# Optimization experiments

Measured on AMD Instinct MI355X. Metric: run time of the kernel, lower is better.

## Reference

```python
import jax, jax.numpy as jnp
import numpy as np
from jax import lax

B, T, HW = 8, 32, 128
D, NH, DEPTH, DFF = 384, 6, 6, 1536
PR = PC = 4
P = PR * PC
EPS = 1e-5


def _ln(x, g, b):
    mu = x.mean(-1, keepdims=True)
    v = ((x - mu) ** 2).mean(-1, keepdims=True)
    return (x - mu) / jnp.sqrt(v + EPS) * g + b


def _conv2d(x, w, s, p):
    return lax.conv_general_dilated(x, w, (s, s), [(p, p), (p, p)],
                                    dimension_numbers=('NCHW', 'OIHW', 'NCHW'))


def _bn(x, g, b, m, v):
    inv = g / jnp.sqrt(v + EPS)
    return x * inv[:, None, None] + (b - m * inv)[:, None, None]


def _gelu(x):
    return jax.nn.gelu(x, approximate=False)


def _forward(frames, conv1_w, bn1_g, bn1_b, bn1_m, bn1_v,
             conv2_w, bn2_g, bn2_b, bn2_m, bn2_v,
             conv3_w, bn3_g, bn3_b, bn3_m, bn3_v, proj_w,
             dw_w, dw_b, pw_w, pw_b, tnorm_g, tnorm_b,
             frame_pos, patch_pos, cls_token, cls_pos,
             qkv_w, qkv_b, out_w, out_b, ln1_g, ln1_b, ln2_g, ln2_b,
             ffn_w1, ffn_b1, ffn_w2, ffn_b2,
             head_ln_g, head_ln_b, head_w1, head_b1, head_w2, head_b2):
    b, t = frames.shape[0], frames.shape[1]
    # ---- FrameEncoder (eval-mode BN) ----
    x = frames.reshape(b * t, 1, HW, HW)
    x = _gelu(_bn(_conv2d(x, conv1_w, 2, 2), bn1_g, bn1_b, bn1_m, bn1_v))
    x = _gelu(_bn(_conv2d(x, conv2_w, 2, 1), bn2_g, bn2_b, bn2_m, bn2_v))
    x = _gelu(_bn(_conv2d(x, conv3_w, 2, 1), bn3_g, bn3_b, bn3_m, bn3_v))
    n, c, hh, ww = x.shape
    # adaptive avg pool (16,16)->(4,4) is an exact 4x4 mean pool
    x = x.reshape(n, c, PR, hh // PR, PC, ww // PC).mean(axis=(3, 5))
    x = jnp.einsum('oc,nchw->nohw', proj_w[:, :, 0, 0], x)  # 1x1 conv proj
    tokens = x.reshape(n, D, P).transpose(0, 2, 1).reshape(b, t, P, D)
    # ---- TemporalConvBlock (per-patch sequences) ----
    tc = tokens.transpose(0, 2, 1, 3).reshape(b * P, t, D)
    out = tc.transpose(0, 2, 1)  # [N, D, t]
    for i, dil in enumerate((1, 2)):
        pad = dil * (3 - 1) // 2
        h = lax.conv_general_dilated(out, dw_w[i], (1,), [(pad, pad)],
                                     rhs_dilation=(dil,), feature_group_count=D,
                                     dimension_numbers=('NCH', 'OIH', 'NCH'))
        h = _gelu(h + dw_b[i][None, :, None])
        h = jnp.einsum('oi,nit->not', pw_w[i], h) + pw_b[i][None, :, None]
        out = h + out
    out = out.transpose(0, 2, 1)
    tc = _ln(out + tc, tnorm_g, tnorm_b)
    tokens = tc.reshape(b, P, t, D).transpose(0, 2, 1, 3)
    # ---- positional + cls ----
    fp = frame_pos[:t].transpose(1, 0, 2)[:, :, None, :]  # [1,t,1,D]
    pp = patch_pos[:, None, :, :]                          # [1,1,P,D]
    tok = (tokens + fp + pp).reshape(b, t * P, D)
    cls = cls_token + cls_pos
    tok = jnp.concatenate([jnp.broadcast_to(cls, (b, 1, D)), tok], axis=1)
    S = t * P + 1
    # ---- block-structured additive mask (faithful to _build_causal_mask) ----
    ids = jnp.repeat(jnp.arange(t), P)
    neg = jnp.finfo(jnp.float32).min
    base = jnp.where(ids[None, :] < ids[:, None], neg, 0.0)
    mask = jnp.zeros((S, S), jnp.float32).at[1:, 1:].set(base).at[1:, 0].set(neg)
    # ---- pre-norm transformer encoder ----
    hd = D // NH
    scale = 1.0 / jnp.sqrt(jnp.float32(hd))
    x = tok
    for i in range(DEPTH):
        h = _ln(x, ln1_g[i], ln1_b[i])
        qkv = h @ qkv_w[i].T + qkv_b[i]
        q, k, v = jnp.split(qkv, 3, axis=-1)
        q = q.reshape(b, S, NH, hd).transpose(0, 2, 1, 3)
        k = k.reshape(b, S, NH, hd).transpose(0, 2, 1, 3)
        v = v.reshape(b, S, NH, hd).transpose(0, 2, 1, 3)
        scores = jnp.einsum('bhqd,bhkd->bhqk', q, k) * scale + mask
        a = jax.nn.softmax(scores, axis=-1)
        o = jnp.einsum('bhqk,bhkd->bhqd', a, v).transpose(0, 2, 1, 3).reshape(b, S, D)
        x = x + (o @ out_w[i].T + out_b[i])
        h2 = _ln(x, ln2_g[i], ln2_b[i])
        x = x + _gelu(h2 @ ffn_w1[i].T + ffn_b1[i]) @ ffn_w2[i].T + ffn_b2[i]
    # ---- coord head ----
    pooled = x[:, 0]
    h = _ln(pooled, head_ln_g, head_ln_b)
    h = _gelu(h @ head_w1.T + head_b1)
    coords = jax.nn.sigmoid(h @ head_w2.T + head_b2)
    return coords


def setup_inputs():
    ks = iter(jax.random.split(jax.random.key(0), 64))

    def r(shape, s):
        return jax.random.normal(next(ks), shape, jnp.float32) * s

    inp = {}
    inp['frames'] = jax.random.normal(next(ks), (B, T, 1, HW, HW), jnp.float32)
    inp['conv1_w'] = r((32, 1, 5, 5), 0.2)
    inp['bn1_g'] = jnp.ones(32); inp['bn1_b'] = jnp.zeros(32)
    inp['bn1_m'] = r((32,), 0.1)
    inp['bn1_v'] = jax.random.uniform(next(ks), (32,), jnp.float32, 0.5, 1.5)
    inp['conv2_w'] = r((64, 32, 3, 3), 0.1)
    inp['bn2_g'] = jnp.ones(64); inp['bn2_b'] = jnp.zeros(64)
    inp['bn2_m'] = r((64,), 0.1)
    inp['bn2_v'] = jax.random.uniform(next(ks), (64,), jnp.float32, 0.5, 1.5)
    inp['conv3_w'] = r((128, 64, 3, 3), 0.07)
    inp['bn3_g'] = jnp.ones(128); inp['bn3_b'] = jnp.zeros(128)
    inp['bn3_m'] = r((128,), 0.1)
    inp['bn3_v'] = jax.random.uniform(next(ks), (128,), jnp.float32, 0.5, 1.5)
    inp['proj_w'] = r((D, 128, 1, 1), 0.08)
    inp['dw_w'] = r((2, D, 1, 3), 0.3)
    inp['dw_b'] = jnp.zeros((2, D))
    inp['pw_w'] = r((2, D, D), 0.05)
    inp['pw_b'] = jnp.zeros((2, D))
    inp['tnorm_g'] = jnp.ones(D); inp['tnorm_b'] = jnp.zeros(D)
    inp['frame_pos'] = r((T, 1, D), 0.02)
    inp['patch_pos'] = r((1, P, D), 0.02)
    inp['cls_token'] = jnp.zeros((1, 1, D))
    inp['cls_pos'] = r((1, 1, D), 0.02)
    inp['qkv_w'] = r((DEPTH, 3 * D, D), 0.02)
    inp['qkv_b'] = jnp.zeros((DEPTH, 3 * D))
    inp['out_w'] = r((DEPTH, D, D), 0.02)
    inp['out_b'] = jnp.zeros((DEPTH, D))
    inp['ln1_g'] = jnp.ones((DEPTH, D)); inp['ln1_b'] = jnp.zeros((DEPTH, D))
    inp['ln2_g'] = jnp.ones((DEPTH, D)); inp['ln2_b'] = jnp.zeros((DEPTH, D))
    inp['ffn_w1'] = r((DEPTH, DFF, D), 0.02)
    inp['ffn_b1'] = jnp.zeros((DEPTH, DFF))
    inp['ffn_w2'] = r((DEPTH, D, DFF), 0.02)
    inp['ffn_b2'] = jnp.zeros((DEPTH, D))
    inp['head_ln_g'] = jnp.ones(D); inp['head_ln_b'] = jnp.zeros(D)
    inp['head_w1'] = r((D, D), 0.02); inp['head_b1'] = jnp.zeros(D)
    inp['head_w2'] = r((2, D), 0.02); inp['head_b2'] = jnp.zeros(2)
    return inp


def reference(frames, conv1_w, bn1_g, bn1_b, bn1_m, bn1_v,
              conv2_w, bn2_g, bn2_b, bn2_m, bn2_v,
              conv3_w, bn3_g, bn3_b, bn3_m, bn3_v, proj_w,
              dw_w, dw_b, pw_w, pw_b, tnorm_g, tnorm_b,
              frame_pos, patch_pos, cls_token, cls_pos,
              qkv_w, qkv_b, out_w, out_b, ln1_g, ln1_b, ln2_g, ln2_b,
              ffn_w1, ffn_b1, ffn_w2, ffn_b2,
              head_ln_g, head_ln_b, head_w1, head_b1, head_w2, head_b2):
    return _forward(frames, conv1_w, bn1_g, bn1_b, bn1_m, bn1_v,
                    conv2_w, bn2_g, bn2_b, bn2_m, bn2_v,
                    conv3_w, bn3_g, bn3_b, bn3_m, bn3_v, proj_w,
                    dw_w, dw_b, pw_w, pw_b, tnorm_g, tnorm_b,
                    frame_pos, patch_pos, cls_token, cls_pos,
                    qkv_w, qkv_b, out_w, out_b, ln1_g, ln1_b, ln2_g, ln2_b,
                    ffn_w1, ffn_b1, ffn_w2, ffn_b2,
                    head_ln_g, head_ln_b, head_w1, head_b1, head_w2, head_b2)
```

## Files before the change

kernel.cpp:

```cpp
#include <hip/hip_runtime.h>
#include <hip/hip_fp16.h>
#include <cstddef>

#define EPSV 1e-5f
#define SPLITS 4

typedef _Float16 f16;
typedef _Float16 f16x8 __attribute__((ext_vector_type(8)));
typedef float f32x4v __attribute__((ext_vector_type(4)));

__device__ __forceinline__ float gelu_f(float x) {
    return 0.5f * x * (1.0f + erff(x * 0.7071067811865476f));
}

__device__ __forceinline__ float gelu_fast(float x) {
    float x2 = x * x;
    float z = x * fmaf(0.10296103f, x2, 2.3025851f);
    float e = exp2f(z);
    float r = __builtin_amdgcn_rcpf(e + 1.0f);
    return fmaf(-x, r, x);
}

__global__ __launch_bounds__(256) void cvt_all_kernel(
    const float* __restrict__ p0, const float* __restrict__ p1,
    const float* __restrict__ p2, const float* __restrict__ p3,
    const float* __restrict__ p4, const float* __restrict__ p5,
    f16* __restrict__ dst)
{
    const int n = 10960896;
    for (int i = blockIdx.x * 256 + threadIdx.x; i < n; i += gridDim.x * 256) {
        const float* s; int off;
        if      (i <   49152) { s = p0; off = i; }
        else if (i <  344064) { s = p1; off = i -   49152; }
        else if (i < 2998272) { s = p2; off = i -  344064; }
        else if (i < 3883008) { s = p3; off = i - 2998272; }
        else if (i < 7421952) { s = p4; off = i - 3883008; }
        else                  { s = p5; off = i - 7421952; }
        dst[i] = (f16)s[off];
    }
}

__global__ __launch_bounds__(256) void conv_w_reorder_kernel(
    const float* __restrict__ w, f16* __restrict__ out, int CO, int CI)
{
    int n = CO * CI * 9;
    for (int i = blockIdx.x * 256 + threadIdx.x; i < n; i += gridDim.x * 256) {
        int t = i % 9; int r = i / 9;
        int ci = r % CI; int co = r / CI;
        out[(size_t)co * CI * 9 + t * CI + ci] = (f16)w[i];
    }
}

__global__ __launch_bounds__(256) void conv1_w_prep_kernel(
    const float* __restrict__ w, const float* __restrict__ g,
    const float* __restrict__ vr, f16* __restrict__ wB)
{
    int i = blockIdx.x * 256 + threadIdx.x;
    if (i >= 1024) return;
    int co = i >> 5, k = i & 31;
    float inv = g[co] * rsqrtf(vr[co] + EPSV);
    wB[i] = (f16)((k < 25) ? w[co * 25 + k] * inv : 0.f);
}

__global__ __launch_bounds__(256) void conv1_mfma_kernel(
    const float* __restrict__ in, const f16* __restrict__ wB,
    const float* __restrict__ bt, const float* __restrict__ mn,
    const float* __restrict__ g, const float* __restrict__ vr,
    f16* __restrict__ out)
{
    __shared__ __align__(16) f16 inpH[35 * 36 + 8];
    __shared__ __align__(16) f16 Bs[32 * 32];
    int bid = blockIdx.x;
    int n = bid >> 4; int tile = bid & 15;
    int ty0 = (tile >> 2) * 16, tx0 = (tile & 3) * 16;
    int t = threadIdx.x;
    const float* ip = in + (size_t)n * 16384;
    for (int e = t; e < 35 * 36; e += 256) {
        int r = e / 36, c = e - r * 36;
        int iy = ty0 * 2 - 2 + r, ix = tx0 * 2 - 2 + c;
        float v = ((unsigned)iy < 128u && (unsigned)ix < 128u && c < 35) ? ip[iy * 128 + ix] : 0.f;
        inpH[e] = (f16)v;
    }
    if (t < 128) {
        int row = t >> 2, seg = (t & 3) * 8;
        *(uint4*)(&Bs[row * 32 + seg]) = *(const uint4*)(wB + row * 32 + seg);
    }
    __syncthreads();
    int w = t >> 6, lane = t & 63;
    int l15 = lane & 15, gq = lane >> 4;
    f16x8 afr[4];
    #pragma unroll
    for (int i = 0; i < 4; i++) {
        int mt = 4 * w + i;
        f16 tmp[8];
        #pragma unroll
        for (int e = 0; e < 8; e++) {
            int kk = 8 * gq + e; if (kk > 24) kk = 24;
            int ky = kk / 5, kx = kk - ky * 5;
            tmp[e] = inpH[(2 * mt + ky) * 36 + 2 * l15 + kx];
        }
        afr[i] = *(f16x8*)tmp;
    }
    f16x8 bfr[2];
    bfr[0] = *(const f16x8*)(&Bs[l15 * 32 + 8 * gq]);
    bfr[1] = *(const f16x8*)(&Bs[(16 + l15) * 32 + 8 * gq]);
    f32x4v zero = {0.f, 0.f, 0.f, 0.f};
    f32x4v acc[4][2];
    #pragma unroll
    for (int i = 0; i < 4; i++) { acc[i][0] = zero; acc[i][1] = zero; }
    #pragma unroll
    for (int i = 0; i < 4; i++) {
        acc[i][0] = __builtin_amdgcn_mfma_f32_16x16x32_f16(afr[i], bfr[0], acc[i][0], 0, 0, 0);
        acc[i][1] = __builtin_amdgcn_mfma_f32_16x16x32_f16(afr[i], bfr[1], acc[i][1], 0, 0, 0);
    }
    float beta[2];
    #pragma unroll
    for (int nt = 0; nt < 2; nt++) {
        int co = nt * 16 + l15;
        float inv = g[co] * rsqrtf(vr[co] + EPSV);
        beta[nt] = bt[co] - mn[co] * inv;
    }
    #pragma unroll
    for (int i = 0; i < 4; i++) {
        int y = ty0 + 4 * w + i;
        #pragma unroll
        for (int q = 0; q < 4; q++) {
            int x = tx0 + 4 * gq + q;
            size_t ob = (((size_t)n * 64 + y) * 64 + x) * 32;
            #pragma unroll
            for (int nt = 0; nt < 2; nt++) {
                int co = nt * 16 + l15;
                out[ob + co] = (f16)gelu_fast(acc[i][nt][q] + beta[nt]);
            }
        }
    }
}

template<int CI, int HI, int CO>
__global__ __launch_bounds__(256) void convg_kernel(
    const f16* __restrict__ in, const f16* __restrict__ wr_,
    const float* __restrict__ g, const float* __restrict__ bt,
    const float* __restrict__ mn, const float* __restrict__ vr,
    f16* __restrict__ out)
{
    constexpr int HO = HI / 2;
    constexpr int HOB = (HO == 32) ? 5 : 4;
    constexpr int K = 9 * CI;
    __shared__ __align__(16) f16 As[64 * 40];
    __shared__ __align__(16) f16 Bs[64 * 40];
    int tid = threadIdx.x;
    int bm = blockIdx.x * 64;
    int bn = blockIdx.y * 64;
    int lrow = tid >> 2, lseg = tid & 3;
    int w = tid >> 6, lane = tid & 63;
    int wr = (w >> 1) * 32, wc = (w & 1) * 32;
    int l15 = lane & 15, l4 = lane >> 4;
    int gp = bm + lrow;
    int pn = gp >> (2 * HOB);
    int prem = gp & ((1 << (2 * HOB)) - 1);
    int oy = prem >> HOB, ox = prem & (HO - 1);

    f32x4v zero = {0.f, 0.f, 0.f, 0.f};
    f32x4v acc[2][2];
    acc[0][0] = zero; acc[0][1] = zero; acc[1][0] = zero; acc[1][1] = zero;

    auto loadTile = [&](int k0, uint4& av, uint4& bv) {
        int tap = k0 / CI;
        int cio = k0 - tap * CI;
        int ky = tap / 3, kx = tap - ky * 3;
        int iy = oy * 2 - 1 + ky, ix = ox * 2 - 1 + kx;
        av = make_uint4(0u, 0u, 0u, 0u);
        if ((unsigned)iy < (unsigned)HI && (unsigned)ix < (unsigned)HI)
            av = *(const uint4*)(in + (((size_t)(pn * HI + iy)) * HI + ix) * CI + cio + lseg * 8);
        bv = *(const uint4*)(wr_ + (size_t)(bn + lrow) * K + k0 + lseg * 8);
    };

    uint4 ra, rb;
    loadTile(0, ra, rb);
    for (int k0 = 0; k0 < K; k0 += 32) {
        __syncthreads();
        *(uint4*)(&As[lrow * 40 + lseg * 8]) = ra;
        *(uint4*)(&Bs[lrow * 40 + lseg * 8]) = rb;
        if (k0 + 32 < K) loadTile(k0 + 32, ra, rb);
        __syncthreads();
        f16x8 a0 = *(const f16x8*)(&As[(wr + l15) * 40 + l4 * 8]);
        f16x8 a1 = *(const f16x8*)(&As[(wr + 16 + l15) * 40 + l4 * 8]);
        f16x8 b0 = *(const f16x8*)(&Bs[(wc + l15) * 40 + l4 * 8]);
        f16x8 b1 = *(const f16x8*)(&Bs[(wc + 16 + l15) * 40 + l4 * 8]);
        acc[0][0] = __builtin_amdgcn_mfma_f32_16x16x32_f16(a0, b0, acc[0][0], 0, 0, 0);
        acc[0][1] = __builtin_amdgcn_mfma_f32_16x16x32_f16(a0, b1, acc[0][1], 0, 0, 0);
        acc[1][0] = __builtin_amdgcn_mfma_f32_16x16x32_f16(a1, b0, acc[1][0], 0, 0, 0);
        acc[1][1] = __builtin_amdgcn_mfma_f32_16x16x32_f16(a1, b1, acc[1][1], 0, 0, 0);
    }
    float inv[2], beta[2];
    #pragma unroll
    for (int ni = 0; ni < 2; ni++) {
        int col = bn + wc + ni * 16 + l15;
        float iv = g[col] * rsqrtf(vr[col] + EPSV);
        inv[ni] = iv; beta[ni] = bt[col] - mn[col] * iv;
    }
    #pragma unroll
    for (int mi = 0; mi < 2; mi++) {
        #pragma unroll
        for (int q = 0; q < 4; q++) {
            int pixel = bm + wr + mi * 16 + l4 * 4 + q;
            #pragma unroll
            for (int ni = 0; ni < 2; ni++) {
                int col = bn + wc + ni * 16 + l15;
                float v = acc[mi][ni][q] * inv[ni] + beta[ni];
                out[(size_t)pixel * CO + col] = (f16)gelu_fast(v);
            }
        }
    }
}

__global__ __launch_bounds__(256) void poolh_kernel(
    const f16* __restrict__ in, f16* __restrict__ out, int NC)
{
    int idx = blockIdx.x * 256 + threadIdx.x;
    if (idx >= NC * 16 * 16) return;
    int cc = idx & 15; int npl = idx >> 4;
    int c0 = cc * 8;
    int n = npl >> 4; int p = npl & 15;
    int ph = p >> 2, pw = p & 3;
    const f16* base = in + (((size_t)(n * 16 + ph * 4)) * 16 + pw * 4) * 128 + c0;
    float s[8] = {};
    #pragma unroll
    for (int dy = 0; dy < 4; dy++)
        #pragma unroll
        for (int dx = 0; dx < 4; dx++) {
            f16x8 v = *(const f16x8*)(base + (dy * 16 + dx) * 128);
            #pragma unroll
            for (int u = 0; u < 8; u++) s[u] += (float)v[u];
        }
    f16* op = out + (size_t)npl * 128 + c0;
    #pragma unroll
    for (int u = 0; u < 8; u++) op[u] = (f16)(s[u] * 0.0625f);
}

template<int OUTF16, int ACT, int VTRANS, int TCMAP>
__global__ __launch_bounds__(256) void gemm_k64_kernel(
    const f16* __restrict__ A, const f16* __restrict__ B,
    const float* __restrict__ bias, const float* __restrict__ res,
    void* __restrict__ Cv, f16* __restrict__ vT, int M, int N, int K, int nrow)
{
    __shared__ __align__(16) f16 As[64 * 72];
    __shared__ __align__(16) f16 Bs[64 * 72];
    int nb = gridDim.x;
    int q = nb >> 3, r = nb & 7;
    int xcd = blockIdx.x & 7, pos = blockIdx.x >> 3;
    int logical = (xcd < r ? xcd * (q + 1) : r * (q + 1) + (xcd - r) * q) + pos;
    int brow = logical % nrow, bcol = logical / nrow;
    int bm = brow * 64, bn = bcol * 64;

    int tid = threadIdx.x;
    int lrow = tid >> 2, lseg = (tid & 3) * 16;
    int w = tid >> 6, lane = tid & 63;
    int wr = (w >> 1) * 32, wc = (w & 1) * 32;
    int l15 = lane & 15, l4 = lane >> 4;
    f32x4v zero = {0.f, 0.f, 0.f, 0.f};
    f32x4v acc[2][2];
    acc[0][0] = zero; acc[0][1] = zero; acc[1][0] = zero; acc[1][1] = zero;

    int arow = bm + lrow;
    bool aok = (arow < M);
    const f16* ap = A + (size_t)arow * K + lseg;
    const f16* bp = B + (size_t)(bn + lrow) * K + lseg;

    uint4 ra0 = make_uint4(0u,0u,0u,0u), ra1 = ra0, rb0, rb1;
    if (aok) { ra0 = *(const uint4*)(ap); ra1 = *(const uint4*)(ap + 8); }
    rb0 = *(const uint4*)(bp); rb1 = *(const uint4*)(bp + 8);

    int nt = K >> 6;
    for (int t = 0; t < nt; t++) {
        __syncthreads();
        *(uint4*)(&As[lrow * 72 + lseg])     = ra0;
        *(uint4*)(&As[lrow * 72 + lseg + 8]) = ra1;
        *(uint4*)(&Bs[lrow * 72 + lseg])     = rb0;
        *(uint4*)(&Bs[lrow * 72 + lseg + 8]) = rb1;
        if (t + 1 < nt) {
            int k0 = (t + 1) << 6;
            if (aok) { ra0 = *(const uint4*)(ap + k0); ra1 = *(const uint4*)(ap + k0 + 8); }
            rb0 = *(const uint4*)(bp + k0); rb1 = *(const uint4*)(bp + k0 + 8);
        }
        __syncthreads();
        #pragma unroll
        for (int s = 0; s < 2; s++) {
            f16x8 a0 = *(const f16x8*)(&As[(wr + l15) * 72 + s * 32 + l4 * 8]);
            f16x8 a1 = *(const f16x8*)(&As[(wr + 16 + l15) * 72 + s * 32 + l4 * 8]);
            f16x8 b0 = *(const f16x8*)(&Bs[(wc + l15) * 72 + s * 32 + l4 * 8]);
            f16x8 b1 = *(const f16x8*)(&Bs[(wc + 16 + l15) * 72 + s * 32 + l4 * 8]);
            acc[0][0] = __builtin_amdgcn_mfma_f32_16x16x32_f16(a0, b0, acc[0][0], 0, 0, 0);
            acc[0][1] = __builtin_amdgcn_mfma_f32_16x16x32_f16(a0, b1, acc[0][1], 0, 0, 0);
            acc[1][0] = __builtin_amdgcn_mfma_f32_16x16x32_f16(a1, b0, acc[1][0], 0, 0, 0);
            acc[1][1] = __builtin_amdgcn_mfma_f32_16x16x32_f16(a1, b1, acc[1][1], 0, 0, 0);
        }
    }

    if (VTRANS && bn >= 768) {
        __syncthreads();
        f16* tile = As;
        #pragma unroll
        for (int mi = 0; mi < 2; mi++)
            #pragma unroll
            for (int qq = 0; qq < 4; qq++) {
                int rl = wr + mi * 16 + l4 * 4 + qq;
                #pragma unroll
                for (int ni = 0; ni < 2; ni++) {
                    int dl = wc + ni * 16 + l15;
                    float v = acc[mi][ni][qq] + bias[bn + dl];
                    tile[dl * 66 + rl] = (f16)v;
                }
            }
        __syncthreads();
        int h = (bn - 768) >> 6;
        int j = tid & 63, dbase = tid >> 6;
        int trow = bm + j;
        if (trow < M) {
            int b = trow / 513;
            int jj = trow - b * 513;
            f16* vb = vT + ((size_t)(b * 6 + h) * 64) * 576 + jj;
            #pragma unroll
            for (int it = 0; it < 16; it++) {
                int d = dbase * 16 + it;
                vb[(size_t)d * 576] = tile[d * 66 + j];
            }
        }
        return;
    }
    #pragma unroll
    for (int mi = 0; mi < 2; mi++) {
        #pragma unroll
        for (int qq = 0; qq < 4; qq++) {
            int row = bm + wr + mi * 16 + l4 * 4 + qq;
            if (row >= M) continue;
            #pragma unroll
            for (int ni = 0; ni < 2; ni++) {
                int col = bn + wc + ni * 16 + l15;
                float v = acc[mi][ni][qq];
                if (bias) v += bias[col];
                if (ACT == 1) v = gelu_fast(v);
                if (res) v += res[(size_t)row * N + col];
                int orow = row;
                if (TCMAP) orow = (row & ~511) | ((row & 15) << 5) | ((row >> 4) & 31);
                if (OUTF16) ((f16*)Cv)[(size_t)orow * N + col] = (f16)v;
                else ((float*)Cv)[(size_t)orow * N + col] = v;
            }
        }
    }
}

template<int ACT>
__global__ __launch_bounds__(256) void gemm_kn128_kernel(
    const f16* __restrict__ A, const f16* __restrict__ B,
    const float* __restrict__ bias, f16* __restrict__ C,
    int M, int N, int K, int nrow)
{
    __shared__ __align__(16) f16 As[64 * 72];
    __shared__ __align__(16) f16 Bs[128 * 72];
    int nb = gridDim.x;
    int q = nb >> 3, r = nb & 7;
    int xcd = blockIdx.x & 7, pos = blockIdx.x >> 3;
    int logical = (xcd < r ? xcd * (q + 1) : r * (q + 1) + (xcd - r) * q) + pos;
    int brow = logical % nrow, bcol = logical / nrow;
    int bm = brow * 64, bn = bcol * 128;

    int tid = threadIdx.x;
    int w = tid >> 6, lane = tid & 63;
    int wr = (w >> 1) * 32, wc = (w & 1) * 64;
    int l15 = lane & 15, l4 = lane >> 4;
    int alrow = tid >> 2, alseg = (tid & 3) * 16;
    int blrow = tid >> 1, blseg = (tid & 1) * 32;

    f32x4v zero = {0.f, 0.f, 0.f, 0.f};
    f32x4v acc[2][4];
    #pragma unroll
    for (int i = 0; i < 2; i++)
        #pragma unroll
        for (int j = 0; j < 4; j++) acc[i][j] = zero;

    int arow = bm + alrow;
    bool aok = (arow < M);
    const f16* ap = A + (size_t)arow * K + alseg;
    const f16* bp = B + (size_t)(bn + blrow) * K + blseg;

    uint4 ra0 = make_uint4(0u,0u,0u,0u), ra1 = ra0;
    uint4 rb0, rb1, rb2, rb3;
    if (aok) { ra0 = *(const uint4*)(ap); ra1 = *(const uint4*)(ap + 8); }
    rb0 = *(const uint4*)(bp);      rb1 = *(const uint4*)(bp + 8);
    rb2 = *(const uint4*)(bp + 16); rb3 = *(const uint4*)(bp + 24);

    int ntiles = K >> 6;
    for (int t = 0; t < ntiles; t++) {
        __syncthreads();
        *(uint4*)(&As[alrow * 72 + alseg])     = ra0;
        *(uint4*)(&As[alrow * 72 + alseg + 8]) = ra1;
        *(uint4*)(&Bs[blrow * 72 + blseg])      = rb0;
        *(uint4*)(&Bs[blrow * 72 + blseg + 8])  = rb1;
        *(uint4*)(&Bs[blrow * 72 + blseg + 16]) = rb2;
        *(uint4*)(&Bs[blrow * 72 + blseg + 24]) = rb3;
        if (t + 1 < ntiles) {
            int k0 = (t + 1) << 6;
            if (aok) { ra0 = *(const uint4*)(ap + k0); ra1 = *(const uint4*)(ap + k0 + 8); }
            rb0 = *(const uint4*)(bp + k0);      rb1 = *(const uint4*)(bp + k0 + 8);
            rb2 = *(const uint4*)(bp + k0 + 16); rb3 = *(const uint4*)(bp + k0 + 24);
        }
        __syncthreads();
        #pragma unroll
        for (int s = 0; s < 2; s++) {
            f16x8 a0 = *(const f16x8*)(&As[(wr + l15) * 72 + s * 32 + l4 * 8]);
            f16x8 a1 = *(const f16x8*)(&As[(wr + 16 + l15) * 72 + s * 32 + l4 * 8]);
            #pragma unroll
            for (int j = 0; j < 4; j++) {
                f16x8 bf = *(const f16x8*)(&Bs[(wc + j * 16 + l15) * 72 + s * 32 + l4 * 8]);
                acc[0][j] = __builtin_amdgcn_mfma_f32_16x16x32_f16(a0, bf, acc[0][j], 0, 0, 0);
                acc[1][j] = __builtin_amdgcn_mfma_f32_16x16x32_f16(a1, bf, acc[1][j], 0, 0, 0);
            }
        }
    }
    #pragma unroll
    for (int mi = 0; mi < 2; mi++) {
        #pragma unroll
        for (int qq = 0; qq < 4; qq++) {
            int row = bm + wr + mi * 16 + l4 * 4 + qq;
            if (row >= M) continue;
            #pragma unroll
            for (int j = 0; j < 4; j++) {
                int col = bn + wc + j * 16 + l15;
                float v = acc[mi][j][qq];
                if (bias) v += bias[col];
                if (ACT == 1) v = gelu_fast(v);
                C[(size_t)row * N + col] = (f16)v;
            }
        }
    }
}

__global__ __launch_bounds__(256) void dwconv_kernel(
    const float* __restrict__ in, const float* __restrict__ w,
    const float* __restrict__ bias, f16* __restrict__ out, int dil)
{
    int idx = blockIdx.x * 256 + threadIdx.x;
    if (idx >= 128 * 32 * 96) return;
    int dg = idx % 96; int t = (idx / 96) & 31; int s = idx / (96 * 32);
    int d = dg * 4;
    const float* ip = in + (size_t)s * 32 * 384 + d;
    float4 acc = *(const float4*)(bias + d);
    #pragma unroll
    for (int k = 0; k < 3; k++) {
        int tt = t + (k - 1) * dil;
        if ((unsigned)tt < 32u) {
            float4 v = *(const float4*)(ip + tt * 384);
            acc.x = fmaf(w[(d + 0) * 3 + k], v.x, acc.x);
            acc.y = fmaf(w[(d + 1) * 3 + k], v.y, acc.y);
            acc.z = fmaf(w[(d + 2) * 3 + k], v.z, acc.z);
            acc.w = fmaf(w[(d + 3) * 3 + k], v.w, acc.w);
        }
    }
    f16 o[4];
    o[0] = (f16)gelu_fast(acc.x); o[1] = (f16)gelu_fast(acc.y);
    o[2] = (f16)gelu_fast(acc.z); o[3] = (f16)gelu_fast(acc.w);
    *(uint2*)(out + ((size_t)(s * 32 + t) * 384 + d)) = *(uint2*)o;
}

__global__ __launch_bounds__(256) void ln_wave_kernel(
    const float* __restrict__ in,
    const float* __restrict__ g, const float* __restrict__ b,
    f16* __restrict__ out, int rows)
{
    int w = threadIdx.x >> 6, lane = threadIdx.x & 63;
    int row = blockIdx.x * 4 + w;
    if (row >= rows) return;
    const float* ip = in + (size_t)row * 384;
    float x[6]; float s = 0.f, s2 = 0.f;
    #pragma unroll
    for (int k = 0; k < 6; k++) {
        float v = ip[lane + 64 * k];
        x[k] = v; s += v; s2 += v * v;
    }
    #pragma unroll
    for (int off = 1; off < 64; off <<= 1) {
        s += __shfl_xor(s, off); s2 += __shfl_xor(s2, off);
    }
    float mu = s * (1.f / 384.f);
    float var = s2 * (1.f / 384.f) - mu * mu;
    float rs = rsqrtf(var + EPSV);
    #pragma unroll
    for (int k = 0; k < 6; k++) {
        int c = lane + 64 * k;
        out[(size_t)row * 384 + c] = (f16)((x[k] - mu) * rs * g[c] + b[c]);
    }
}

__global__ __launch_bounds__(128) void build_x_kernel(
    const float* __restrict__ mix, const float* __restrict__ tc,
    const float* __restrict__ tg, const float* __restrict__ tb,
    const float* __restrict__ fpos, const float* __restrict__ ppos,
    float* __restrict__ x)
{
    int row = blockIdx.x;
    int t = row & 31; int bp = row >> 5;
    int p = bp & 15; int b = bp >> 4;
    int tid = threadIdx.x;
    const float* ip = mix + (size_t)row * 384;
    const float* ip2 = tc + (size_t)row * 384;
    __shared__ float red[128], red2[128];
    float v[3]; float s = 0.f, s2 = 0.f;
    #pragma unroll
    for (int j = 0; j < 3; j++) {
        float val = ip[tid + 128 * j] + ip2[tid + 128 * j];
        v[j] = val; s += val; s2 += val * val;
    }
    red[tid] = s; red2[tid] = s2; __syncthreads();
    for (int off = 64; off >= 1; off >>= 1) {
        if (tid < off) { red[tid] += red[tid + off]; red2[tid] += red2[tid + off]; }
        __syncthreads();
    }
    float mu = red[0] * (1.f / 384.f);
    float var = red2[0] * (1.f / 384.f) - mu * mu;
    float rs = rsqrtf(var + EPSV);
    size_t xbase = ((size_t)b * 513 + 1 + t * 16 + p) * 384;
    #pragma unroll
    for (int j = 0; j < 3; j++) {
        int c = tid + 128 * j;
        float y = (v[j] - mu) * rs * tg[c] + tb[c] + fpos[t * 384 + c] + ppos[p * 384 + c];
        x[xbase + c] = y;
    }
}

__global__ __launch_bounds__(256) void cls_kernel(
    const float* __restrict__ ct, const float* __restrict__ cp, float* __restrict__ x)
{
    int idx = blockIdx.x * 256 + threadIdx.x;
    if (idx >= 8 * 384) return;
    int c = idx % 384; int b = idx / 384;
    x[(size_t)b * 513 * 384 + c] = ct[c] + cp[c];
}

__global__ __launch_bounds__(256) void fattn_split_kernel(
    const f16* __restrict__ qkv, const f16* __restrict__ vT,
    f16* __restrict__ Op, float* __restrict__ ml)
{
    __shared__ __align__(16) f16 Pl[4][16][72];
    int qt = blockIdx.x;
    int bh = blockIdx.y; int h = bh % 6; int b = bh / 6;
    int third = blockIdx.z;
    int tid = threadIdx.x;
    int w = tid >> 6, lane = tid & 63;
    int l15 = lane & 15, g = lane >> 4;
    int q0w = qt * 64 + w * 16;
    if (q0w > 512) return;
    const size_t RS = 1152;
    const f16* qbase = qkv + (size_t)b * 513 * RS + h * 64;
    const f16* kbase = qbase + 384;
    const f16* vtb = vT + (size_t)bh * 64 * 576;

    f16x8 qf[2];
    {
        int qrow = q0w + l15; if (qrow > 512) qrow = 512;
        const f16* qp = qbase + (size_t)qrow * RS + g * 8;
        qf[0] = *(const f16x8*)(qp);
        qf[1] = *(const f16x8*)(qp + 32);
    }

    f32x4v zero = {0.f, 0.f, 0.f, 0.f};
    f32x4v O[4]; float m[4], l[4];
    #pragma unroll
    for (int i = 0; i < 4; i++) { O[i] = zero; m[i] = -INFINITY; l[i] = 0.f; }

    int jt0 = 0;
    if (q0w > 0) { int fmin = (q0w - 1) >> 4; jt0 = (fmin * 16 + 1) >> 6; }

    int jrow[4];
    #pragma unroll
    for (int jf = 0; jf < 4; jf++) jrow[jf] = jf * 16 + l15;

    auto loadK = [&](int j0, f16x8* kr) {
        #pragma unroll
        for (int s = 0; s < 2; s++)
            #pragma unroll
            for (int jf = 0; jf < 4; jf++) {
                int j = j0 + jrow[jf]; if (j > 512) j = 512;
                kr[s * 4 + jf] = *(const f16x8*)(kbase + (size_t)j * RS + s * 32 + g * 8);
            }
    };

    int jt = jt0 + third;
    f16x8 kreg[8];
    if (jt < 9) loadK(jt * 64, kreg);

    for (; jt < 9; jt += SPLITS) {
        int j0 = jt * 64;
        f16x8 vreg[8];
        #pragma unroll
        for (int s = 0; s < 2; s++)
            #pragma unroll
            for (int df = 0; df < 4; df++)
                vreg[s * 4 + df] = *(const f16x8*)(vtb + (size_t)(df * 16 + l15) * 576 + j0 + s * 32 + g * 8);
        f32x4v S[4];
        #pragma unroll
        for (int jf = 0; jf < 4; jf++) S[jf] = zero;
        #pragma unroll
        for (int s = 0; s < 2; s++)
            #pragma unroll
            for (int jf = 0; jf < 4; jf++)
                S[jf] = __builtin_amdgcn_mfma_f32_16x16x32_f16(qf[s], kreg[s * 4 + jf], S[jf], 0, 0, 0);
        f16x8 knext[8];
        if (jt + SPLITS < 9) loadK((jt + SPLITS) * 64, knext);
        float pj[4][4];
        #pragma unroll
        for (int r = 0; r < 4; r++) {
            int qi = q0w + 4 * g + r;
            int fi = (qi == 0) ? -1 : ((qi - 1) >> 4);
            float mx = -INFINITY;
            #pragma unroll
            for (int jf = 0; jf < 4; jf++) {
                int j = j0 + jrow[jf];
                bool valid = (qi < 513) && (j < 513) &&
                             !((qi != 0) && ((j == 0) || (((j - 1) >> 4) < fi)));
                float sv = valid ? S[jf][r] * 0.125f : -INFINITY;
                pj[jf][r] = sv;
                mx = fmaxf(mx, sv);
            }
            mx = fmaxf(mx, __shfl_xor(mx, 1));
            mx = fmaxf(mx, __shfl_xor(mx, 2));
            mx = fmaxf(mx, __shfl_xor(mx, 4));
            mx = fmaxf(mx, __shfl_xor(mx, 8));
            float mn = fmaxf(m[r], mx);
            float alpha = (m[r] == -INFINITY) ? 0.f : __expf(m[r] - mn);
            float ls = 0.f;
            #pragma unroll
            for (int jf = 0; jf < 4; jf++) {
                float p = (pj[jf][r] == -INFINITY) ? 0.f : __expf(pj[jf][r] - mn);
                pj[jf][r] = p; ls += p;
            }
            ls += __shfl_xor(ls, 1); ls += __shfl_xor(ls, 2);
            ls += __shfl_xor(ls, 4); ls += __shfl_xor(ls, 8);
            l[r] = alpha * l[r] + ls;
            m[r] = mn;
            #pragma unroll
            for (int df = 0; df < 4; df++) O[df][r] *= alpha;
        }
        #pragma unroll
        for (int jf = 0; jf < 4; jf++)
            #pragma unroll
            for (int r = 0; r < 4; r++)
                Pl[w][4 * g + r][jf * 16 + l15] = (f16)pj[jf][r];
        #pragma unroll
        for (int s = 0; s < 2; s++) {
            f16x8 pf = *(const f16x8*)(&Pl[w][l15][s * 32 + g * 8]);
            #pragma unroll
            for (int df = 0; df < 4; df++)
                O[df] = __builtin_amdgcn_mfma_f32_16x16x32_f16(pf, vreg[s * 4 + df], O[df], 0, 0, 0);
        }
        #pragma unroll
        for (int i = 0; i < 8; i++) kreg[i] = knext[i];
    }

    int rowbase = third * 24624 + bh * 513;
    #pragma unroll
    for (int r = 0; r < 4; r++) {
        int qi = q0w + 4 * g + r;
        if (qi > 512) continue;
        size_t ro = (size_t)(rowbase + qi);
        #pragma unroll
        for (int df = 0; df < 4; df++)
            Op[ro * 64 + df * 16 + l15] = (f16)O[df][r];
        if (l15 == 0) {
            ml[ro * 2 + 0] = m[r];
            ml[ro * 2 + 1] = l[r];
        }
    }
}

__global__ __launch_bounds__(256) void attn_combine_kernel(
    const f16* __restrict__ Op, const float* __restrict__ ml,
    f16* __restrict__ ob)
{
    int row = blockIdx.x * 4 + (threadIdx.x >> 6);
    if (row >= 24624) return;
    int lane = threadIdx.x & 63;
    int bh = row / 513, qi = row - bh * 513;
    int b = bh / 6, h = bh - b * 6;
    float mv[SPLITS], lv[SPLITS], mm = -INFINITY;
    #pragma unroll
    for (int s = 0; s < SPLITS; s++) {
        mv[s] = ml[((size_t)s * 24624 + row) * 2];
        lv[s] = ml[((size_t)s * 24624 + row) * 2 + 1];
        mm = fmaxf(mm, mv[s]);
    }
    float onum = 0.f, lden = 0.f;
    #pragma unroll
    for (int s = 0; s < SPLITS; s++) {
        float a = (mv[s] == -INFINITY) ? 0.f : __expf(mv[s] - mm);
        lden += lv[s] * a;
        onum += (float)Op[((size_t)s * 24624 + row) * 64 + lane] * a;
    }
    ob[((size_t)(b * 513 + qi)) * 384 + h * 64 + lane] = (f16)(onum / lden);
}

__global__ __launch_bounds__(384) void head_kernel(
    const float* __restrict__ x, const float* __restrict__ lg, const float* __restrict__ lb,
    const float* __restrict__ w1, const float* __restrict__ b1,
    const float* __restrict__ w2, const float* __restrict__ b2,
    float* __restrict__ out)
{
    int b = blockIdx.x; int t = threadIdx.x;
    __shared__ float hs[384], h1[384];
    __shared__ float rs[6], rs2[6];
    const float* xp = x + (size_t)b * 513 * 384;
    float v = xp[t];
    float s = v, s2 = v * v;
    #pragma unroll
    for (int off = 32; off >= 1; off >>= 1) {
        s += __shfl_down(s, off); s2 += __shfl_down(s2, off);
    }
    if ((t & 63) == 0) { rs[t >> 6] = s; rs2[t >> 6] = s2; }
    __syncthreads();
    float S = 0.f, S2 = 0.f;
    #pragma unroll
    for (int i = 0; i < 6; i++) { S += rs[i]; S2 += rs2[i]; }
    float mu = S * (1.f / 384.f);
    float var = S2 * (1.f / 384.f) - mu * mu;
    float rstd = rsqrtf(var + EPSV);
    hs[t] = (v - mu) * rstd * lg[t] + lb[t];
    __syncthreads();
    const float* wr = w1 + (size_t)t * 384;
    float acc = b1[t];
    for (int c = 0; c < 384; c += 4) {
        float4 w4 = *reinterpret_cast<const float4*>(wr + c);
        acc += w4.x * hs[c] + w4.y * hs[c + 1] + w4.z * hs[c + 2] + w4.w * hs[c + 3];
    }
    h1[t] = gelu_f(acc);
    __syncthreads();
    float p0 = h1[t] * w2[t], p1 = h1[t] * w2[384 + t];
    #pragma unroll
    for (int off = 32; off >= 1; off >>= 1) {
        p0 += __shfl_down(p0, off); p1 += __shfl_down(p1, off);
    }
    if ((t & 63) == 0) { rs[t >> 6] = p0; rs2[t >> 6] = p1; }
    __syncthreads();
    if (t == 0) {
        float a0 = b2[0], a1 = b2[1];
        #pragma unroll
        for (int i = 0; i < 6; i++) { a0 += rs[i]; a1 += rs2[i]; }
        out[b * 2 + 0] = 1.f / (1.f + expf(-a0));
        out[b * 2 + 1] = 1.f / (1.f + expf(-a1));
    }
}

static inline int cdiv(int a, int b) { return (a + b - 1) / b; }

extern "C" void kernel_launch(void* const* d_in, const int* in_sizes, int n_in,
                              void* d_out, int out_size, void* d_ws, size_t ws_size,
                              hipStream_t stream)
{
    const float* frames  = (const float*)d_in[0];
    const float* conv1_w = (const float*)d_in[1];
    const float* bn1_g = (const float*)d_in[2]; const float* bn1_b = (const float*)d_in[3];
    const float* bn1_m = (const float*)d_in[4]; const float* bn1_v = (const float*)d_in[5];
    const float* conv2_w = (const float*)d_in[6];
    const float* bn2_g = (const float*)d_in[7]; const float* bn2_b = (const float*)d_in[8];
    const float* bn2_m = (const float*)d_in[9]; const float* bn2_v = (const float*)d_in[10];
    const float* conv3_w = (const float*)d_in[11];
    const float* bn3_g = (const float*)d_in[12]; const float* bn3_b = (const float*)d_in[13];
    const float* bn3_m = (const float*)d_in[14]; const float* bn3_v = (const float*)d_in[15];
    const float* proj_w = (const float*)d_in[16];
    const float* dw_w = (const float*)d_in[17]; const float* dw_b = (const float*)d_in[18];
    const float* pw_w = (const float*)d_in[19]; const float* pw_b = (const float*)d_in[20];
    const float* tnorm_g = (const float*)d_in[21]; const float* tnorm_b = (const float*)d_in[22];
    const float* frame_pos = (const float*)d_in[23];
    const float* patch_pos = (const float*)d_in[24];
    const float* cls_token = (const float*)d_in[25];
    const float* cls_pos = (const float*)d_in[26];
    const float* qkv_w = (const float*)d_in[27]; const float* qkv_b = (const float*)d_in[28];
    const float* out_w = (const float*)d_in[29]; const float* out_b = (const float*)d_in[30];
    const float* ln1_g = (const float*)d_in[31]; const float* ln1_b = (const float*)d_in[32];
    const float* ln2_g = (const float*)d_in[33]; const float* ln2_b = (const float*)d_in[34];
    const float* ffn_w1 = (const float*)d_in[35]; const float* ffn_b1 = (const float*)d_in[36];
    const float* ffn_w2 = (const float*)d_in[37]; const float* ffn_b2 = (const float*)d_in[38];
    const float* head_ln_g = (const float*)d_in[39]; const float* head_ln_b = (const float*)d_in[40];
    const float* head_w1 = (const float*)d_in[41]; const float* head_b1 = (const float*)d_in[42];
    const float* head_w2 = (const float*)d_in[43]; const float* head_b2 = (const float*)d_in[44];
    (void)in_sizes; (void)n_in; (void)out_size; (void)ws_size;

    char* base = (char*)d_ws;
    size_t off = 0;
    auto alloc = [&](size_t bytes) { void* p = base + off; off = (off + bytes + 255) & ~(size_t)255; return p; };

    f16* wtotal = (f16*)alloc((size_t)10960896 * 2);
    f16* projw16 = wtotal;
    f16* pw16    = wtotal + 49152;
    f16* qkvw16  = wtotal + 344064;
    f16* outw16  = wtotal + 2998272;
    f16* f1w16   = wtotal + 3883008;
    f16* f2w16   = wtotal + 7421952;
    f16* c1wB    = (f16*)alloc(1024 * 2);
    f16* c2w16   = (f16*)alloc((size_t)64 * 288 * 2);
    f16* c3w16   = (f16*)alloc((size_t)128 * 576 * 2);
    f16* pooled  = (f16*)alloc((size_t)4096 * 128 * 2);
    float* tc    = (float*)alloc((size_t)4096 * 384 * 4);

    size_t ustart = off;
    f16* c1h = (f16*)alloc((size_t)256 * 64 * 64 * 32 * 2);
    f16* c2h = (f16*)alloc((size_t)256 * 32 * 32 * 64 * 2);
    f16* c3h = (f16*)alloc((size_t)256 * 16 * 16 * 128 * 2);
    size_t uend_stem = off;
    off = ustart;
    float* mA = (float*)alloc((size_t)4096 * 384 * 4);
    float* mB = (float*)alloc((size_t)4096 * 384 * 4);
    f16*   mh = (f16*)alloc((size_t)4096 * 384 * 2);
    float* xb   = (float*)alloc((size_t)8 * 513 * 384 * 4);
    f16*   hb   = (f16*)alloc((size_t)8 * 513 * 384 * 2);
    f16*   qkvb = (f16*)alloc((size_t)8 * 513 * 1152 * 2);
    f16*   vTb  = (f16*)alloc((size_t)48 * 64 * 576 * 2);
    f16*   ob   = (f16*)alloc((size_t)8 * 513 * 384 * 2);
    f16*   ffb  = (f16*)alloc((size_t)8 * 513 * 1536 * 2);
    f16*   Opart = (f16*)alloc((size_t)SPLITS * 24624 * 64 * 2);
    float* mlpart = (float*)alloc((size_t)SPLITS * 24624 * 2 * 4);
    if (off < uend_stem) off = uend_stem;

    cvt_all_kernel<<<4096, 256, 0, stream>>>(
        proj_w, pw_w, qkv_w, out_w, ffn_w1, ffn_w2, wtotal);
    conv1_w_prep_kernel<<<4, 256, 0, stream>>>(conv1_w, bn1_g, bn1_v, c1wB);
    conv_w_reorder_kernel<<<cdiv(64 * 288, 256), 256, 0, stream>>>(conv2_w, c2w16, 64, 32);
    conv_w_reorder_kernel<<<cdiv(128 * 576, 256), 256, 0, stream>>>(conv3_w, c3w16, 128, 64);

    conv1_mfma_kernel<<<256 * 16, 256, 0, stream>>>(
        frames, c1wB, bn1_b, bn1_m, bn1_g, bn1_v, c1h);
    convg_kernel<32, 64, 64><<<dim3(4096, 1), 256, 0, stream>>>(
        c1h, c2w16, bn2_g, bn2_b, bn2_m, bn2_v, c2h);
    convg_kernel<64, 32, 128><<<dim3(1024, 2), 256, 0, stream>>>(
        c2h, c3w16, bn3_g, bn3_b, bn3_m, bn3_v, c3h);
    poolh_kernel<<<256, 256, 0, stream>>>(c3h, pooled, 256);
    gemm_k64_kernel<0, 0, 0, 1><<<384, 256, 0, stream>>>(
        pooled, projw16, nullptr, nullptr, tc, nullptr, 4096, 384, 128, 64);

    dwconv_kernel<<<cdiv(128 * 32 * 96, 256), 256, 0, stream>>>(
        tc, dw_w, dw_b, mh, 1);
    gemm_k64_kernel<0, 0, 0, 0><<<384, 256, 0, stream>>>(
        mh, pw16, pw_b, tc, mA, nullptr, 4096, 384, 384, 64);
    dwconv_kernel<<<cdiv(128 * 32 * 96, 256), 256, 0, stream>>>(
        mA, dw_w + 384 * 3, dw_b + 384, mh, 2);
    gemm_k64_kernel<0, 0, 0, 0><<<384, 256, 0, stream>>>(
        mh, pw16 + 384 * 384, pw_b + 384, mA, mB, nullptr, 4096, 384, 384, 64);

    build_x_kernel<<<128 * 32, 128, 0, stream>>>(
        mB, tc, tnorm_g, tnorm_b, frame_pos, patch_pos, xb);
    cls_kernel<<<cdiv(8 * 384, 256), 256, 0, stream>>>(cls_token, cls_pos, xb);

    const int M = 8 * 513;
    const int NR = cdiv(M, 64);
    for (int l = 0; l < 6; l++) {
        ln_wave_kernel<<<cdiv(M, 4), 256, 0, stream>>>(xb,
            ln1_g + (size_t)l * 384, ln1_b + (size_t)l * 384, hb, M);
        gemm_k64_kernel<1, 0, 1, 0><<<NR * 18, 256, 0, stream>>>(
            hb, qkvw16 + (size_t)l * 1152 * 384, qkv_b + (size_t)l * 1152,
            nullptr, qkvb, vTb, M, 1152, 384, NR);
        fattn_split_kernel<<<dim3(9, 48, SPLITS), 256, 0, stream>>>(qkvb, vTb, Opart, mlpart);
        attn_combine_kernel<<<cdiv(24624, 4), 256, 0, stream>>>(Opart, mlpart, ob);
        gemm_k64_kernel<0, 0, 0, 0><<<NR * 6, 256, 0, stream>>>(
            ob, outw16 + (size_t)l * 384 * 384, out_b + (size_t)l * 384,
            xb, xb, nullptr, M, 384, 384, NR);
        ln_wave_kernel<<<cdiv(M, 4), 256, 0, stream>>>(xb,
            ln2_g + (size_t)l * 384, ln2_b + (size_t)l * 384, hb, M);
        gemm_kn128_kernel<1><<<NR * 12, 256, 0, stream>>>(
            hb, f1w16 + (size_t)l * 1536 * 384, ffn_b1 + (size_t)l * 1536,
            ffb, M, 1536, 384, NR);
        gemm_k64_kernel<0, 0, 0, 0><<<NR * 6, 256, 0, stream>>>(
            ffb, f2w16 + (size_t)l * 384 * 1536, ffn_b2 + (size_t)l * 384,
            xb, xb, nullptr, M, 384, 1536, NR);
    }

    head_kernel<<<8, 384, 0, stream>>>(
        xb, head_ln_g, head_ln_b, head_w1, head_b1, head_w2, head_b2, (float*)d_out);
}
```

Before: 834.3 us.

## Merge weight-prep kernels, pack conv1 stores, vectorize LayerNorm and build_x

Four weight-preparation launches are merged into one grid-stride prep kernel. Conv1's output channels are permuted in the weight buffer so each lane writes two adjacent f16 channels as one 32-bit store. The LayerNorm and build_x kernels now use float2 loads and stores, and build_x uses one wave per row with shuffle reductions instead of a shared-memory tree with many barriers. The aim is less launch overhead and fewer, wider memory transactions in small memory-bound kernels.

```diff
diff --git a/kernel.cpp b/kernel.cpp
--- a/kernel.cpp
+++ b/kernel.cpp
@@ -21,45 +21,48 @@
     return fmaf(-x, r, x);
 }
 
-__global__ __launch_bounds__(256) void cvt_all_kernel(
+__global__ __launch_bounds__(256) void prep_all_kernel(
     const float* __restrict__ p0, const float* __restrict__ p1,
     const float* __restrict__ p2, const float* __restrict__ p3,
     const float* __restrict__ p4, const float* __restrict__ p5,
-    f16* __restrict__ dst)
-{
-    const int n = 10960896;
-    for (int i = blockIdx.x * 256 + threadIdx.x; i < n; i += gridDim.x * 256) {
-        const float* s; int off;
-        if      (i <   49152) { s = p0; off = i; }
-        else if (i <  344064) { s = p1; off = i -   49152; }
-        else if (i < 2998272) { s = p2; off = i -  344064; }
-        else if (i < 3883008) { s = p3; off = i - 2998272; }
-        else if (i < 7421952) { s = p4; off = i - 3883008; }
-        else                  { s = p5; off = i - 7421952; }
-        dst[i] = (f16)s[off];
-    }
-}
-
-__global__ __launch_bounds__(256) void conv_w_reorder_kernel(
-    const float* __restrict__ w, f16* __restrict__ out, int CO, int CI)
-{
-    int n = CO * CI * 9;
-    for (int i = blockIdx.x * 256 + threadIdx.x; i < n; i += gridDim.x * 256) {
-        int t = i % 9; int r = i / 9;
-        int ci = r % CI; int co = r / CI;
-        out[(size_t)co * CI * 9 + t * CI + ci] = (f16)w[i];
-    }
-}
-
-__global__ __launch_bounds__(256) void conv1_w_prep_kernel(
-    const float* __restrict__ w, const float* __restrict__ g,
-    const float* __restrict__ vr, f16* __restrict__ wB)
-{
-    int i = blockIdx.x * 256 + threadIdx.x;
-    if (i >= 1024) return;
-    int co = i >> 5, k = i & 31;
-    float inv = g[co] * rsqrtf(vr[co] + EPSV);
-    wB[i] = (f16)((k < 25) ? w[co * 25 + k] * inv : 0.f);
+    f16* __restrict__ dst,
+    const float* __restrict__ c1w, const float* __restrict__ bn1g,
+    const float* __restrict__ bn1v, f16* __restrict__ c1wB,
+    const float* __restrict__ c2w, f16* __restrict__ c2o,
+    const float* __restrict__ c3w, f16* __restrict__ c3o)
+{
+    const int n0 = 10960896;
+    const int n1 = n0 + 1024;
+    const int n2 = n1 + 64 * 288;
+    const int n3 = n2 + 128 * 576;
+    for (int i = blockIdx.x * 256 + threadIdx.x; i < n3; i += gridDim.x * 256) {
+        if (i < n0) {
+            const float* s; int off;
+            if      (i <   49152) { s = p0; off = i; }
+            else if (i <  344064) { s = p1; off = i -   49152; }
+            else if (i < 2998272) { s = p2; off = i -  344064; }
+            else if (i < 3883008) { s = p3; off = i - 2998272; }
+            else if (i < 7421952) { s = p4; off = i - 3883008; }
+            else                  { s = p5; off = i - 7421952; }
+            dst[i] = (f16)s[off];
+        } else if (i < n1) {
+            int j = i - n0;
+            int r = j >> 5, k = j & 31;
+            int co = ((r & 15) << 1) | (r >> 4);
+            float inv = bn1g[co] * rsqrtf(bn1v[co] + EPSV);
+            c1wB[j] = (f16)((k < 25) ? c1w[co * 25 + k] * inv : 0.f);
+        } else if (i < n2) {
+            int j = i - n1;
+            int t = j % 9; int r = j / 9;
+            int ci = r % 32; int co = r / 32;
+            c2o[(size_t)co * 288 + t * 32 + ci] = (f16)c2w[j];
+        } else {
+            int j = i - n2;
+            int t = j % 9; int r = j / 9;
+            int ci = r % 64; int co = r / 64;
+            c3o[(size_t)co * 576 + t * 64 + ci] = (f16)c3w[j];
+        }
+    }
 }
 
 __global__ __launch_bounds__(256) void conv1_mfma_kernel(
@@ -116,7 +119,7 @@
     float beta[2];
     #pragma unroll
     for (int nt = 0; nt < 2; nt++) {
-        int co = nt * 16 + l15;
+        int co = 2 * l15 + nt;
         float inv = g[co] * rsqrtf(vr[co] + EPSV);
         beta[nt] = bt[co] - mn[co] * inv;
     }
@@ -126,12 +129,11 @@
         #pragma unroll
         for (int q = 0; q < 4; q++) {
             int x = tx0 + 4 * gq + q;
-            size_t ob = (((size_t)n * 64 + y) * 64 + x) * 32;
-            #pragma unroll
-            for (int nt = 0; nt < 2; nt++) {
-                int co = nt * 16 + l15;
-                out[ob + co] = (f16)gelu_fast(acc[i][nt][q] + beta[nt]);
-            }
+            size_t ob = (((size_t)n * 64 + y) * 64 + x) * 32 + 2 * l15;
+            f16 o2[2];
+            o2[0] = (f16)gelu_fast(acc[i][0][q] + beta[0]);
+            o2[1] = (f16)gelu_fast(acc[i][1][q] + beta[1]);
+            *(uint*)(out + ob) = *(uint*)o2;
         }
     }
 }
@@ -472,11 +474,12 @@
     int row = blockIdx.x * 4 + w;
     if (row >= rows) return;
     const float* ip = in + (size_t)row * 384;
-    float x[6]; float s = 0.f, s2 = 0.f;
-    #pragma unroll
-    for (int k = 0; k < 6; k++) {
-        float v = ip[lane + 64 * k];
-        x[k] = v; s += v; s2 += v * v;
+    float2 x2[3]; float s = 0.f, s2 = 0.f;
+    #pragma unroll
+    for (int k = 0; k < 3; k++) {
+        float2 v = *(const float2*)(ip + lane * 2 + 128 * k);
+        x2[k] = v;
+        s += v.x + v.y; s2 += v.x * v.x + v.y * v.y;
     }
     #pragma unroll
     for (int off = 1; off < 64; off <<= 1) {
@@ -486,45 +489,59 @@
     float var = s2 * (1.f / 384.f) - mu * mu;
     float rs = rsqrtf(var + EPSV);
     #pragma unroll
-    for (int k = 0; k < 6; k++) {
-        int c = lane + 64 * k;
-        out[(size_t)row * 384 + c] = (f16)((x[k] - mu) * rs * g[c] + b[c]);
-    }
-}
-
-__global__ __launch_bounds__(128) void build_x_kernel(
+    for (int k = 0; k < 3; k++) {
+        int c = lane * 2 + 128 * k;
+        float2 gg = *(const float2*)(g + c);
+        float2 bb = *(const float2*)(b + c);
+        f16 o[2];
+        o[0] = (f16)((x2[k].x - mu) * rs * gg.x + bb.x);
+        o[1] = (f16)((x2[k].y - mu) * rs * gg.y + bb.y);
+        *(uint*)(out + (size_t)row * 384 + c) = *(uint*)o;
+    }
+}
+
+__global__ __launch_bounds__(256) void build_x_kernel(
     const float* __restrict__ mix, const float* __restrict__ tc,
     const float* __restrict__ tg, const float* __restrict__ tb,
     const float* __restrict__ fpos, const float* __restrict__ ppos,
     float* __restrict__ x)
 {
-    int row = blockIdx.x;
+    int w = threadIdx.x >> 6, lane = threadIdx.x & 63;
+    int row = blockIdx.x * 4 + w;
+    if (row >= 4096) return;
     int t = row & 31; int bp = row >> 5;
     int p = bp & 15; int b = bp >> 4;
-    int tid = threadIdx.x;
     const float* ip = mix + (size_t)row * 384;
     const float* ip2 = tc + (size_t)row * 384;
-    __shared__ float red[128], red2[128];
-    float v[3]; float s = 0.f, s2 = 0.f;
-    #pragma unroll
-    for (int j = 0; j < 3; j++) {
-        float val = ip[tid + 128 * j] + ip2[tid + 128 * j];
-        v[j] = val; s += val; s2 += val * val;
-    }
-    red[tid] = s; red2[tid] = s2; __syncthreads();
-    for (int off = 64; off >= 1; off >>= 1) {
-        if (tid < off) { red[tid] += red[tid + off]; red2[tid] += red2[tid + off]; }
-        __syncthreads();
-    }
-    float mu = red[0] * (1.f / 384.f);
-    float var = red2[0] * (1.f / 384.f) - mu * mu;
+    float2 v2[3]; float s = 0.f, s2 = 0.f;
+    #pragma unroll
+    for (int k = 0; k < 3; k++) {
+        int c = lane * 2 + 128 * k;
+        float2 a = *(const float2*)(ip + c);
+        float2 bb = *(const float2*)(ip2 + c);
+        float2 v = make_float2(a.x + bb.x, a.y + bb.y);
+        v2[k] = v;
+        s += v.x + v.y; s2 += v.x * v.x + v.y * v.y;
+    }
+    #pragma unroll
+    for (int off = 1; off < 64; off <<= 1) {
+        s += __shfl_xor(s, off); s2 += __shfl_xor(s2, off);
+    }
+    float mu = s * (1.f / 384.f);
+    float var = s2 * (1.f / 384.f) - mu * mu;
     float rs = rsqrtf(var + EPSV);
     size_t xbase = ((size_t)b * 513 + 1 + t * 16 + p) * 384;
     #pragma unroll
-    for (int j = 0; j < 3; j++) {
-        int c = tid + 128 * j;
-        float y = (v[j] - mu) * rs * tg[c] + tb[c] + fpos[t * 384 + c] + ppos[p * 384 + c];
-        x[xbase + c] = y;
+    for (int k = 0; k < 3; k++) {
+        int c = lane * 2 + 128 * k;
+        float2 gg = *(const float2*)(tg + c);
+        float2 bb = *(const float2*)(tb + c);
+        float2 fp = *(const float2*)(fpos + t * 384 + c);
+        float2 pp = *(const float2*)(ppos + p * 384 + c);
+        float2 y;
+        y.x = (v2[k].x - mu) * rs * gg.x + bb.x + fp.x + pp.x;
+        y.y = (v2[k].y - mu) * rs * gg.y + bb.y + fp.y + pp.y;
+        *(float2*)(x + xbase + c) = y;
     }
 }
 
@@ -820,11 +837,9 @@
     float* mlpart = (float*)alloc((size_t)SPLITS * 24624 * 2 * 4);
     if (off < uend_stem) off = uend_stem;
 
-    cvt_all_kernel<<<4096, 256, 0, stream>>>(
-        proj_w, pw_w, qkv_w, out_w, ffn_w1, ffn_w2, wtotal);
-    conv1_w_prep_kernel<<<4, 256, 0, stream>>>(conv1_w, bn1_g, bn1_v, c1wB);
-    conv_w_reorder_kernel<<<cdiv(64 * 288, 256), 256, 0, stream>>>(conv2_w, c2w16, 64, 32);
-    conv_w_reorder_kernel<<<cdiv(128 * 576, 256), 256, 0, stream>>>(conv3_w, c3w16, 128, 64);
+    prep_all_kernel<<<4096, 256, 0, stream>>>(
+        proj_w, pw_w, qkv_w, out_w, ffn_w1, ffn_w2, wtotal,
+        conv1_w, bn1_g, bn1_v, c1wB, conv2_w, c2w16, conv3_w, c3w16);
 
     conv1_mfma_kernel<<<256 * 16, 256, 0, stream>>>(
         frames, c1wB, bn1_b, bn1_m, bn1_g, bn1_v, c1h);
@@ -845,7 +860,7 @@
     gemm_k64_kernel<0, 0, 0, 0><<<384, 256, 0, stream>>>(
         mh, pw16 + 384 * 384, pw_b + 384, mA, mB, nullptr, 4096, 384, 384, 64);
 
-    build_x_kernel<<<128 * 32, 128, 0, stream>>>(
+    build_x_kernel<<<1024, 256, 0, stream>>>(
         mB, tc, tnorm_g, tnorm_b, frame_pos, patch_pos, xb);
     cls_kernel<<<cdiv(8 * 384, 256), 256, 0, stream>>>(cls_token, cls_pos, xb);
 
```

After: 830.2 us, median of 2. No clear change (-0.5%).
